# Kernel optimization log

Measured on AMD Instinct MI355X. Metric: run time of the kernel, lower is better.

Reference implementation:

```python
import jax, jax.numpy as jnp
import numpy as np

B, S, H = 1, 2048, 2048
NH, NKV, HD = 32, 8, 64
GROUPS = NH // NKV
ROPE_BASE = 10000.0
NEG = -1e9


def setup_inputs() -> dict:
    key = jax.random.key(0)
    ks = jax.random.split(key, 5)
    hidden_states = jax.random.normal(ks[0], (B, S, H), dtype=jnp.float32)
    # causal additive mask: 0 on/below diagonal, large negative above
    causal = jnp.tril(jnp.ones((S, S), dtype=bool))
    attention_mask = jnp.where(causal, 0.0, NEG).astype(jnp.float32)[None, None]
    position_ids = jnp.arange(S, dtype=jnp.int64)[None, :].astype(jnp.int32)
    sc = 1.0 / np.sqrt(H)
    Wq = jax.random.normal(ks[1], (NH * HD, H), dtype=jnp.float32) * sc
    Wk = jax.random.normal(ks[2], (NKV * HD, H), dtype=jnp.float32) * sc
    Wv = jax.random.normal(ks[3], (NKV * HD, H), dtype=jnp.float32) * sc
    Wo = jax.random.normal(ks[4], (H, H), dtype=jnp.float32) * sc
    return {"hidden_states": hidden_states, "attention_mask": attention_mask,
            "position_ids": position_ids, "Wq": Wq, "Wk": Wk, "Wv": Wv, "Wo": Wo}


def _rotate_half(x):
    x1, x2 = jnp.split(x, 2, axis=-1)
    return jnp.concatenate((-x2, x1), axis=-1)


def _rope_cos_sin(position_ids, dtype):
    inv_freq = 1.0 / (ROPE_BASE ** (jnp.arange(0, HD, 2, dtype=jnp.float32) / HD))
    # [b, s, hd/2]
    freqs = position_ids.astype(jnp.float32)[:, :, None] * inv_freq[None, None, :]
    emb = jnp.concatenate((freqs, freqs), axis=-1)  # [b, s, hd]
    # unsqueeze head dim -> [b, 1, s, hd]
    return jnp.cos(emb).astype(dtype)[:, None], jnp.sin(emb).astype(dtype)[:, None]


def reference(hidden_states, attention_mask, position_ids, Wq, Wk, Wv, Wo):
    b, s, _ = hidden_states.shape
    q = (hidden_states @ Wq.T).reshape(b, s, NH, HD).transpose(0, 2, 1, 3)
    k = (hidden_states @ Wk.T).reshape(b, s, NKV, HD).transpose(0, 2, 1, 3)
    v = (hidden_states @ Wv.T).reshape(b, s, NKV, HD).transpose(0, 2, 1, 3)

    cos, sin = _rope_cos_sin(position_ids, hidden_states.dtype)
    q = q * cos + _rotate_half(q) * sin
    k = k * cos + _rotate_half(k) * sin

    # GQA: duplicate KV heads (repeat_interleave along head dim)
    k = jnp.repeat(k, GROUPS, axis=1)
    v = jnp.repeat(v, GROUPS, axis=1)

    scale = 1.0 / jnp.sqrt(jnp.asarray(HD, dtype=hidden_states.dtype))
    scores = jnp.einsum('bhqd,bhkd->bhqk', q, k) * scale + attention_mask
    attn = jax.nn.softmax(scores, axis=-1)
    out = jnp.einsum('bhqk,bhkd->bhqd', attn, v)
    out = out.transpose(0, 2, 1, 3).reshape(b, s, NH * HD)
    return out @ Wo.T
```

## Files before the change

### kernel.cpp

```cpp
#include <hip/hip_runtime.h>
#include <math.h>

#define S_LEN 2048
#define HID   2048
#define NH    32
#define NKV   8
#define HD    64
#define BK    32

typedef short short4x __attribute__((ext_vector_type(4)));
typedef short short8  __attribute__((ext_vector_type(8)));
typedef float floatx4 __attribute__((ext_vector_type(4)));

static __device__ __forceinline__ ushort f2bf(float f) {
  unsigned u = __float_as_uint(f);
  u += 0x7fffu + ((u >> 16) & 1u);
  return (ushort)(u >> 16);
}

static __device__ __forceinline__ void gl2lds16(const ushort* g, ushort* l) {
  __builtin_amdgcn_global_load_lds(
      (const __attribute__((address_space(1))) unsigned int*)g,
      (__attribute__((address_space(3))) unsigned int*)l, 16, 0, 0);
}

#define QH  1048576
#define QW  1048576
#define QKq  262144
#define QVq  262144
#define QO  1048576
__global__ void cvt_all_kernel(const float* __restrict__ h,
                               const float* __restrict__ wq,
                               const float* __restrict__ wk,
                               const float* __restrict__ wv,
                               const float* __restrict__ wo,
                               ushort* __restrict__ hb,
                               ushort* __restrict__ wqkvb,
                               ushort* __restrict__ wob) {
  int idx = blockIdx.x * 256 + threadIdx.x;
  const float* src; ushort* dst; int so, dqo;
  if (idx < QH)                    { src = h;  dst = hb;    so = idx;                   dqo = so; }
  else if (idx < QH + QW)          { src = wq; dst = wqkvb; so = idx - QH;              dqo = so; }
  else if (idx < QH + QW + QKq)    { src = wk; dst = wqkvb; so = idx - QH - QW;         dqo = so + QW; }
  else if (idx < QH + QW + QKq + QVq) { src = wv; dst = wqkvb; so = idx - QH - QW - QKq; dqo = so + QW + QKq; }
  else                             { src = wo; dst = wob;   so = idx - QH - QW - QKq - QVq; dqo = so; }
  float4 v = ((const float4*)src)[so];
  ushort4 o;
  o.x = f2bf(v.x); o.y = f2bf(v.y); o.z = f2bf(v.z); o.w = f2bf(v.w);
  ((ushort4*)dst)[dqo] = o;
}

__global__ __launch_bounds__(256) void gemm64_bt_kernel(
    const ushort* __restrict__ A, const ushort* __restrict__ B,
    float* __restrict__ C, int M, int N, int K) {
  __shared__ __align__(16) ushort As[128 * BK];
  __shared__ __align__(16) ushort Bs[64 * BK];

  const int tid  = threadIdx.x;
  const int wave = tid >> 6;
  const int lane = tid & 63;
  const int r16  = lane & 15;
  const int quad = lane >> 4;

  const int m_base = blockIdx.y * 128;
  const int n_base = blockIdx.x * 64;
  const int wm = wave * 32;

  const int lrow = lane >> 2;
  const int scol = (lane & 3) * 8;
  const ushort* ag0 = A + (size_t)(m_base + wave * 32 + lrow) * K + scol;
  const ushort* ag1 = ag0 + (size_t)16 * K;
  const ushort* bg  = B + (size_t)(n_base + wave * 16 + lrow) * K + scol;
  ushort* as0 = As + (wave * 32) * BK;
  ushort* as1 = As + (wave * 32 + 16) * BK;
  ushort* bs  = Bs + (wave * 16) * BK;

  floatx4 acc[2][4];
#pragma unroll
  for (int i = 0; i < 2; ++i)
#pragma unroll
    for (int j = 0; j < 4; ++j) acc[i][j] = floatx4{0.f, 0.f, 0.f, 0.f};

  for (int kk = 0; kk < K; kk += BK) {
    __syncthreads();
    gl2lds16(ag0 + kk, as0);
    gl2lds16(ag1 + kk, as1);
    gl2lds16(bg + kk, bs);
    __syncthreads();

    short8 af[2], bf[4];
#pragma unroll
    for (int i = 0; i < 2; ++i)
      af[i] = *(const short8*)&As[(wm + i * 16 + r16) * BK + quad * 8];
#pragma unroll
    for (int j = 0; j < 4; ++j)
      bf[j] = *(const short8*)&Bs[(j * 16 + r16) * BK + quad * 8];
#pragma unroll
    for (int i = 0; i < 2; ++i)
#pragma unroll
      for (int j = 0; j < 4; ++j)
        acc[i][j] = __builtin_amdgcn_mfma_f32_16x16x32_bf16(af[i], bf[j], acc[i][j], 0, 0, 0);
  }

#pragma unroll
  for (int i = 0; i < 2; ++i)
#pragma unroll
    for (int j = 0; j < 4; ++j) {
      const int cm = m_base + wm + i * 16 + quad * 4;
      const int cn = n_base + j * 16 + r16;
#pragma unroll
      for (int r = 0; r < 4; ++r)
        C[(size_t)(cm + r) * N + cn] = acc[i][j][r];
    }
}

__global__ __launch_bounds__(256) void gemm_qkv_kernel(
    const ushort* __restrict__ A, const ushort* __restrict__ B,
    const int* __restrict__ pos,
    ushort* __restrict__ qr,
    ushort* __restrict__ kr,
    ushort* __restrict__ vtb) {
  __shared__ __align__(16) ushort As[128 * BK];
  __shared__ __align__(16) ushort Bs[64 * BK];

  const int K = HID;
  const int tid  = threadIdx.x;
  const int wave = tid >> 6;
  const int lane = tid & 63;
  const int r16  = lane & 15;
  const int quad = lane >> 4;

  const int m_base = blockIdx.y * 128;
  const int n_base = blockIdx.x * 64;
  const int wm = wave * 32;

  const int lrow = lane >> 2;
  const int scol = (lane & 3) * 8;
  const ushort* ag0 = A + (size_t)(m_base + wave * 32 + lrow) * K + scol;
  const ushort* ag1 = ag0 + (size_t)16 * K;
  const ushort* bg  = B + (size_t)(n_base + wave * 16 + lrow) * K + scol;
  ushort* as0 = As + (wave * 32) * BK;
  ushort* as1 = As + (wave * 32 + 16) * BK;
  ushort* bs  = Bs + (wave * 16) * BK;

  floatx4 acc[2][4];
#pragma unroll
  for (int i = 0; i < 2; ++i)
#pragma unroll
    for (int j = 0; j < 4; ++j) acc[i][j] = floatx4{0.f, 0.f, 0.f, 0.f};

  for (int kk = 0; kk < K; kk += BK) {
    __syncthreads();
    gl2lds16(ag0 + kk, as0);
    gl2lds16(ag1 + kk, as1);
    gl2lds16(bg + kk, bs);
    __syncthreads();

    short8 af[2], bf[4];
#pragma unroll
    for (int i = 0; i < 2; ++i)
      af[i] = *(const short8*)&As[(wm + i * 16 + r16) * BK + quad * 8];
#pragma unroll
    for (int j = 0; j < 4; ++j)
      bf[j] = *(const short8*)&Bs[(j * 16 + r16) * BK + quad * 8];
#pragma unroll
    for (int i = 0; i < 2; ++i)
#pragma unroll
      for (int j = 0; j < 4; ++j)
        acc[i][j] = __builtin_amdgcn_mfma_f32_16x16x32_bf16(af[i], bf[j], acc[i][j], 0, 0, 0);
  }

  const int n0 = n_base;
  if (n0 < HID + NKV * HD) {
    ushort* dst;
    if (n0 < HID) dst = qr + (size_t)(n0 >> 6) * S_LEN * 64;
    else          dst = kr + (size_t)((n0 - HID) >> 6) * S_LEN * 64;
    const float invfA = powf(10000.0f, -(float)r16 * (1.0f / 32.0f));
    const float invfB = powf(10000.0f, -(float)(16 + r16) * (1.0f / 32.0f));
#pragma unroll
    for (int i = 0; i < 2; ++i) {
#pragma unroll
      for (int r = 0; r < 4; ++r) {
        const int s = m_base + wm + i * 16 + quad * 4 + r;
        const float p = (float)pos[s];
        float snA, csA, snB, csB;
        sincosf(p * invfA, &snA, &csA);
        sincosf(p * invfB, &snB, &csB);
        ushort* row = dst + (size_t)s * 64;
        row[r16]      = f2bf(acc[i][0][r] * csA - acc[i][2][r] * snA);
        row[16 + r16] = f2bf(acc[i][1][r] * csB - acc[i][3][r] * snB);
        row[32 + r16] = f2bf(acc[i][2][r] * csA + acc[i][0][r] * snA);
        row[48 + r16] = f2bf(acc[i][3][r] * csB + acc[i][1][r] * snB);
      }
    }
  } else {
    const int hh = (n0 - HID - NKV * HD) >> 6;
#pragma unroll
    for (int i = 0; i < 2; ++i) {
      const int s0 = m_base + wm + i * 16 + quad * 4;
#pragma unroll
      for (int j = 0; j < 4; ++j) {
        const int d = j * 16 + r16;
        ushort4 o4;
        o4.x = f2bf(acc[i][j][0]);
        o4.y = f2bf(acc[i][j][1]);
        o4.z = f2bf(acc[i][j][2]);
        o4.w = f2bf(acc[i][j][3]);
        *(ushort4*)&vtb[((size_t)hh * 64 + d) * S_LEN + s0] = o4;
      }
    }
  }
}

#define LOG2E_SC 0.180336880f
#define MSTAT    16.0f

__global__ __launch_bounds__(256) void attn_kernel(
    const ushort* __restrict__ Q,
    const ushort* __restrict__ K,
    const ushort* __restrict__ Vt,
    ushort* __restrict__ O) {
  __shared__ __align__(16) ushort Ks[64][72];
  __shared__ __align__(16) ushort Vs[64][72];
  __shared__ __align__(16) ushort Pw[4][16][72];

  const int h    = blockIdx.x;
  const int kh   = h >> 2;
  const int y    = blockIdx.y;
  const int qt   = (y & 1) ? (31 - (y >> 1)) : (y >> 1);
  const int tid  = threadIdx.x;
  const int wave = tid >> 6;
  const int lane = tid & 63;
  const int r16  = lane & 15;
  const int quad = lane >> 4;

  const int q_glob = qt * 64 + wave * 16 + r16;

  const ushort* qp = Q + ((size_t)h * S_LEN + q_glob) * 64 + quad * 8;
  const short8 qf0 = *(const short8*)qp;
  const short8 qf1 = *(const short8*)(qp + 32);

  float l = 0.f;
  floatx4 oacc[4];
#pragma unroll
  for (int n = 0; n < 4; ++n) oacc[n] = floatx4{0.f, 0.f, 0.f, 0.f};

  for (int kt = 0; kt <= qt; ++kt) {
    __syncthreads();
    {
      const ushort* ksrc = K  + ((size_t)kh * S_LEN + kt * 64) * 64;
      const ushort* vsrc = Vt + ((size_t)kh * 64) * S_LEN + kt * 64;
#pragma unroll
      for (int i = tid; i < 512; i += 256) {
        int r = i >> 3, c = (i & 7) * 8;
        *(short8*)&Ks[r][c] = *(const short8*)(ksrc + (size_t)r * 64 + c);
        *(short8*)&Vs[r][c] = *(const short8*)(vsrc + (size_t)r * S_LEN + c);
      }
    }
    __syncthreads();

    floatx4 sacc[4];
#pragma unroll
    for (int t = 0; t < 4; ++t) {
      short8 kf0 = *(const short8*)&Ks[t * 16 + r16][quad * 8];
      short8 kf1 = *(const short8*)&Ks[t * 16 + r16][32 + quad * 8];
      floatx4 z = {0.f, 0.f, 0.f, 0.f};
      z = __builtin_amdgcn_mfma_f32_16x16x32_bf16(kf0, qf0, z, 0, 0, 0);
      sacc[t] = __builtin_amdgcn_mfma_f32_16x16x32_bf16(kf1, qf1, z, 0, 0, 0);
    }

    const bool diag = (kt == qt);
    const int key0 = kt * 64 + quad * 4;
    float ps = 0.f;
#pragma unroll
    for (int t = 0; t < 4; ++t) {
      float p[4];
#pragma unroll
      for (int r = 0; r < 4; ++r) {
        float sc = sacc[t][r] * LOG2E_SC - MSTAT;
        if (diag && (key0 + t * 16 + r) > q_glob) sc = -1e30f;
        p[r] = __builtin_amdgcn_exp2f(sc);
      }
      ps += (p[0] + p[1]) + (p[2] + p[3]);
      *(short4x*)&Pw[wave][r16][t * 16 + quad * 4] =
          short4x{(short)f2bf(p[0]), (short)f2bf(p[1]),
                  (short)f2bf(p[2]), (short)f2bf(p[3])};
    }
    l += ps;

    short8 pf0 = *(const short8*)&Pw[wave][r16][quad * 8];
    short8 pf1 = *(const short8*)&Pw[wave][r16][32 + quad * 8];
#pragma unroll
    for (int n = 0; n < 4; ++n) {
      short8 vf0 = *(const short8*)&Vs[n * 16 + r16][quad * 8];
      short8 vf1 = *(const short8*)&Vs[n * 16 + r16][32 + quad * 8];
      oacc[n] = __builtin_amdgcn_mfma_f32_16x16x32_bf16(vf0, pf0, oacc[n], 0, 0, 0);
      oacc[n] = __builtin_amdgcn_mfma_f32_16x16x32_bf16(vf1, pf1, oacc[n], 0, 0, 0);
    }
  }

  l += __shfl_xor(l, 16);
  l += __shfl_xor(l, 32);
  const float inv_l = 1.f / l;
#pragma unroll
  for (int n = 0; n < 4; ++n) {
    ushort4 o4;
    o4.x = f2bf(oacc[n][0] * inv_l);
    o4.y = f2bf(oacc[n][1] * inv_l);
    o4.z = f2bf(oacc[n][2] * inv_l);
    o4.w = f2bf(oacc[n][3] * inv_l);
    *(ushort4*)&O[(size_t)q_glob * (NH * HD) + h * 64 + n * 16 + quad * 4] = o4;
  }
}

extern "C" void kernel_launch(void* const* d_in, const int* in_sizes, int n_in,
                              void* d_out, int out_size, void* d_ws, size_t ws_size,
                              hipStream_t stream) {
  const float* hidden = (const float*)d_in[0];
  const int*   pos    = (const int*)d_in[2];
  const float* Wq     = (const float*)d_in[3];
  const float* Wk     = (const float*)d_in[4];
  const float* Wv     = (const float*)d_in[5];
  const float* Wo     = (const float*)d_in[6];
  float* out = (float*)d_out;

  const int NQKV = HID + 2 * NKV * HD;

  char* w = (char*)d_ws;
  auto carve = [&](size_t bytes) { char* p = w; w += bytes; return p; };
  ushort* hb    = (ushort*)carve((size_t)S_LEN * HID * 2);
  ushort* wqkvb = (ushort*)carve((size_t)NQKV * HID * 2);
  ushort* wob   = (ushort*)carve((size_t)HID * HID * 2);
  ushort* qr    = (ushort*)carve((size_t)NH * S_LEN * HD * 2);
  ushort* kr    = (ushort*)carve((size_t)NKV * S_LEN * HD * 2);
  ushort* vtb   = (ushort*)carve((size_t)NKV * HD * S_LEN * 2);
  ushort* ob    = (ushort*)carve((size_t)S_LEN * HID * 2);

  cvt_all_kernel<<<(QH + QW + QKq + QVq + QO) / 256, 256, 0, stream>>>(
      hidden, Wq, Wk, Wv, Wo, hb, wqkvb, wob);

  dim3 gqkv(NQKV / 64, S_LEN / 128);
  gemm_qkv_kernel<<<gqkv, 256, 0, stream>>>(hb, wqkvb, pos, qr, kr, vtb);

  dim3 ga(NH, S_LEN / 64);
  attn_kernel<<<ga, 256, 0, stream>>>(qr, kr, vtb, ob);

  dim3 go(HID / 64, S_LEN / 128);
  gemm64_bt_kernel<<<go, 256, 0, stream>>>(ob, wob, out, S_LEN, HID, HID);
}
```

Before: 256.2 us.

## Remap GEMM blocks for XCD-aware locality and load two KV tiles per sync

Both GEMM kernels now launch on a 1D grid and derive block coordinates so that each of 8 blockIdx residues (likely mapping to the 8 XCDs) gets two consecutive M-row bands. The intent is better L2 reuse of A rows within an XCD. The attention kernel now loads two 64-key K/V tiles per barrier pair into doubled LDS buffers, halving the number of syncs per query tile. The cost is twice the LDS for K/V, which may lower occupancy. The mapping also assumes the M-tile count is exactly 16.

```diff
diff --git a/kernel.cpp b/kernel.cpp
--- a/kernel.cpp
+++ b/kernel.cpp
@@ -52,9 +52,14 @@
 
 __global__ __launch_bounds__(256) void gemm64_bt_kernel(
     const ushort* __restrict__ A, const ushort* __restrict__ B,
-    float* __restrict__ C, int M, int N, int K) {
+    float* __restrict__ C, int M, int N, int K, int gx) {
   __shared__ __align__(16) ushort As[128 * BK];
   __shared__ __align__(16) ushort Bs[64 * BK];
+
+  const int g  = blockIdx.x & 7;
+  const int s  = blockIdx.x >> 3;
+  const int by = g * 2 + s / gx;
+  const int bx = s % gx;
 
   const int tid  = threadIdx.x;
   const int wave = tid >> 6;
@@ -62,8 +67,8 @@
   const int r16  = lane & 15;
   const int quad = lane >> 4;
 
-  const int m_base = blockIdx.y * 128;
-  const int n_base = blockIdx.x * 64;
+  const int m_base = by * 128;
+  const int n_base = bx * 64;
   const int wm = wave * 32;
 
   const int lrow = lane >> 2;
@@ -119,9 +124,15 @@
     const int* __restrict__ pos,
     ushort* __restrict__ qr,
     ushort* __restrict__ kr,
-    ushort* __restrict__ vtb) {
+    ushort* __restrict__ vtb,
+    int gx) {
   __shared__ __align__(16) ushort As[128 * BK];
   __shared__ __align__(16) ushort Bs[64 * BK];
+
+  const int g  = blockIdx.x & 7;
+  const int s_ = blockIdx.x >> 3;
+  const int by = g * 2 + s_ / gx;
+  const int bx = s_ % gx;
 
   const int K = HID;
   const int tid  = threadIdx.x;
@@ -130,8 +141,8 @@
   const int r16  = lane & 15;
   const int quad = lane >> 4;
 
-  const int m_base = blockIdx.y * 128;
-  const int n_base = blockIdx.x * 64;
+  const int m_base = by * 128;
+  const int n_base = bx * 64;
   const int wm = wave * 32;
 
   const int lrow = lane >> 2;
@@ -220,8 +231,8 @@
     const ushort* __restrict__ K,
     const ushort* __restrict__ Vt,
     ushort* __restrict__ O) {
-  __shared__ __align__(16) ushort Ks[64][72];
-  __shared__ __align__(16) ushort Vs[64][72];
+  __shared__ __align__(16) ushort Ks[2][64][72];
+  __shared__ __align__(16) ushort Vs[2][64][72];
   __shared__ __align__(16) ushort Pw[4][16][72];
 
   const int h    = blockIdx.x;
@@ -245,57 +256,66 @@
 #pragma unroll
   for (int n = 0; n < 4; ++n) oacc[n] = floatx4{0.f, 0.f, 0.f, 0.f};
 
-  for (int kt = 0; kt <= qt; ++kt) {
+  for (int t0 = 0; t0 <= qt; t0 += 2) {
     __syncthreads();
     {
-      const ushort* ksrc = K  + ((size_t)kh * S_LEN + kt * 64) * 64;
-      const ushort* vsrc = Vt + ((size_t)kh * 64) * S_LEN + kt * 64;
-#pragma unroll
-      for (int i = tid; i < 512; i += 256) {
-        int r = i >> 3, c = (i & 7) * 8;
-        *(short8*)&Ks[r][c] = *(const short8*)(ksrc + (size_t)r * 64 + c);
-        *(short8*)&Vs[r][c] = *(const short8*)(vsrc + (size_t)r * S_LEN + c);
-      }
-    }
-    __syncthreads();
-
-    floatx4 sacc[4];
-#pragma unroll
-    for (int t = 0; t < 4; ++t) {
-      short8 kf0 = *(const short8*)&Ks[t * 16 + r16][quad * 8];
-      short8 kf1 = *(const short8*)&Ks[t * 16 + r16][32 + quad * 8];
-      floatx4 z = {0.f, 0.f, 0.f, 0.f};
-      z = __builtin_amdgcn_mfma_f32_16x16x32_bf16(kf0, qf0, z, 0, 0, 0);
-      sacc[t] = __builtin_amdgcn_mfma_f32_16x16x32_bf16(kf1, qf1, z, 0, 0, 0);
-    }
-
-    const bool diag = (kt == qt);
-    const int key0 = kt * 64 + quad * 4;
-    float ps = 0.f;
-#pragma unroll
-    for (int t = 0; t < 4; ++t) {
-      float p[4];
-#pragma unroll
-      for (int r = 0; r < 4; ++r) {
-        float sc = sacc[t][r] * LOG2E_SC - MSTAT;
-        if (diag && (key0 + t * 16 + r) > q_glob) sc = -1e30f;
-        p[r] = __builtin_amdgcn_exp2f(sc);
-      }
-      ps += (p[0] + p[1]) + (p[2] + p[3]);
-      *(short4x*)&Pw[wave][r16][t * 16 + quad * 4] =
-          short4x{(short)f2bf(p[0]), (short)f2bf(p[1]),
-                  (short)f2bf(p[2]), (short)f2bf(p[3])};
-    }
-    l += ps;
-
-    short8 pf0 = *(const short8*)&Pw[wave][r16][quad * 8];
-    short8 pf1 = *(const short8*)&Pw[wave][r16][32 + quad * 8];
-#pragma unroll
-    for (int n = 0; n < 4; ++n) {
-      short8 vf0 = *(const short8*)&Vs[n * 16 + r16][quad * 8];
-      short8 vf1 = *(const short8*)&Vs[n * 16 + r16][32 + quad * 8];
-      oacc[n] = __builtin_amdgcn_mfma_f32_16x16x32_bf16(vf0, pf0, oacc[n], 0, 0, 0);
-      oacc[n] = __builtin_amdgcn_mfma_f32_16x16x32_bf16(vf1, pf1, oacc[n], 0, 0, 0);
+      const ushort* ksrc = K  + ((size_t)kh * S_LEN + t0 * 64) * 64;
+      const ushort* vsrc = Vt + ((size_t)kh * 64) * S_LEN + t0 * 64;
+      for (int i = tid; i < 1024; i += 256) {
+        int half = i >> 9;
+        int j = i & 511;
+        int r = j >> 3, c = (j & 7) * 8;
+        *(short8*)&Ks[half][r][c] =
+            *(const short8*)(ksrc + (size_t)(half * 64 + r) * 64 + c);
+        *(short8*)&Vs[half][r][c] =
+            *(const short8*)(vsrc + (size_t)r * S_LEN + half * 64 + c);
+      }
+    }
+    __syncthreads();
+
+    const int hmax = (t0 + 1 <= qt) ? 2 : 1;
+#pragma unroll 1
+    for (int half = 0; half < hmax; ++half) {
+      const int kt = t0 + half;
+
+      floatx4 sacc[4];
+#pragma unroll
+      for (int t = 0; t < 4; ++t) {
+        short8 kf0 = *(const short8*)&Ks[half][t * 16 + r16][quad * 8];
+        short8 kf1 = *(const short8*)&Ks[half][t * 16 + r16][32 + quad * 8];
+        floatx4 z = {0.f, 0.f, 0.f, 0.f};
+        z = __builtin_amdgcn_mfma_f32_16x16x32_bf16(kf0, qf0, z, 0, 0, 0);
+        sacc[t] = __builtin_amdgcn_mfma_f32_16x16x32_bf16(kf1, qf1, z, 0, 0, 0);
+      }
+
+      const bool diag = (kt == qt);
+      const int key0 = kt * 64 + quad * 4;
+      float ps = 0.f;
+#pragma unroll
+      for (int t = 0; t < 4; ++t) {
+        float p[4];
+#pragma unroll
+        for (int r = 0; r < 4; ++r) {
+          float sc = sacc[t][r] * LOG2E_SC - MSTAT;
+          if (diag && (key0 + t * 16 + r) > q_glob) sc = -1e30f;
+          p[r] = __builtin_amdgcn_exp2f(sc);
+        }
+        ps += (p[0] + p[1]) + (p[2] + p[3]);
+        *(short4x*)&Pw[wave][r16][t * 16 + quad * 4] =
+            short4x{(short)f2bf(p[0]), (short)f2bf(p[1]),
+                    (short)f2bf(p[2]), (short)f2bf(p[3])};
+      }
+      l += ps;
+
+      short8 pf0 = *(const short8*)&Pw[wave][r16][quad * 8];
+      short8 pf1 = *(const short8*)&Pw[wave][r16][32 + quad * 8];
+#pragma unroll
+      for (int n = 0; n < 4; ++n) {
+        short8 vf0 = *(const short8*)&Vs[half][n * 16 + r16][quad * 8];
+        short8 vf1 = *(const short8*)&Vs[half][n * 16 + r16][32 + quad * 8];
+        oacc[n] = __builtin_amdgcn_mfma_f32_16x16x32_bf16(vf0, pf0, oacc[n], 0, 0, 0);
+        oacc[n] = __builtin_amdgcn_mfma_f32_16x16x32_bf16(vf1, pf1, oacc[n], 0, 0, 0);
+      }
     }
   }
 
@@ -339,12 +359,12 @@
   cvt_all_kernel<<<(QH + QW + QKq + QVq + QO) / 256, 256, 0, stream>>>(
       hidden, Wq, Wk, Wv, Wo, hb, wqkvb, wob);
 
-  dim3 gqkv(NQKV / 64, S_LEN / 128);
-  gemm_qkv_kernel<<<gqkv, 256, 0, stream>>>(hb, wqkvb, pos, qr, kr, vtb);
+  gemm_qkv_kernel<<<(NQKV / 64) * (S_LEN / 128), 256, 0, stream>>>(
+      hb, wqkvb, pos, qr, kr, vtb, NQKV / 64);
 
   dim3 ga(NH, S_LEN / 64);
   attn_kernel<<<ga, 256, 0, stream>>>(qr, kr, vtb, ob);
 
-  dim3 go(HID / 64, S_LEN / 128);
-  gemm64_bt_kernel<<<go, 256, 0, stream>>>(ob, wob, out, S_LEN, HID, HID);
-}
+  gemm64_bt_kernel<<<(HID / 64) * (S_LEN / 128), 256, 0, stream>>>(
+      ob, wob, out, S_LEN, HID, HID, HID / 64);
+}
```

Result: faster. 246.7 us (-3.7%).
